# Kernel tuning notes

Hardware: AMD Instinct MI355X
Metric: run time of the kernel (lower is better)

Reference implementation:

```python
import jax, jax.numpy as jnp
import numpy as np

N_NODES = 100000


def gcn_layer(x, row, col, W, b, n):
    # x: [N, Fin] -> h: [N, Fout]
    h = x @ W + b
    deg = jax.ops.segment_sum(jnp.ones_like(row, dtype=h.dtype), row, num_segments=n)
    dis = deg ** -0.5  # deg >= 1 thanks to self loops
    norm = dis[row] * dis[col]          # [E]
    msg = norm[:, None] * h[row]        # gather + scale
    return jax.ops.segment_sum(msg, col, num_segments=n)  # scatter-add to targets


def setup_inputs() -> dict:
    key = jax.random.key(0)
    k1, k2, k3, k4, k5, k6 = jax.random.split(key, 6)
    x = jax.random.normal(k1, (N_NODES, 512), dtype=jnp.float32)
    edge_index = jax.random.randint(k2, (2, 3200000), 0, N_NODES, dtype=jnp.int32)
    W1 = jax.random.normal(k3, (512, 16), dtype=jnp.float32) * 0.05
    b1 = jax.random.normal(k4, (16,), dtype=jnp.float32) * 0.05
    W2 = jax.random.normal(k5, (16, 40), dtype=jnp.float32) * 0.05
    b2 = jax.random.normal(k6, (40,), dtype=jnp.float32) * 0.05
    return {"x": x, "edge_index": edge_index, "W1": W1, "b1": b1, "W2": W2, "b2": b2}


def reference(x, edge_index, W1, b1, W2, b2):
    n = x.shape[0]
    # add_self_loops
    loops = jnp.arange(n, dtype=edge_index.dtype)
    row = jnp.concatenate([edge_index[0], loops])
    col = jnp.concatenate([edge_index[1], loops])
    h = gcn_layer(x, row, col, W1, b1, n)
    h = jax.nn.relu(h)
    # F.dropout with training=False (eval) is identity
    h = gcn_layer(h, row, col, W2, b2, n)
    return jax.nn.log_softmax(h, axis=1)
```

## Files before the change

### kernel.cpp

```cpp
#include <hip/hip_runtime.h>
#include <math.h>

#define N_NODES 100000
#define N_EDGES 3200000
#define F_IN    512
#define F1      16
#define F2      40

#define N_BUCKETS 6250
#define CAP       768

#define BR 256
#define KK 32
#define XPITCH 36

__global__ __launch_bounds__(256, 4) void mm1_kernel(
        const float* __restrict__ x, const float* __restrict__ W1,
        const float* __restrict__ b1, const float* __restrict__ dis,
        float* __restrict__ h1t) {
    __shared__ float xs[BR * XPITCH];
    __shared__ float ws[KK * F1];
    int t = threadIdx.x;
    int rbase = blockIdx.x * BR;
    int jq = t & 3;
    int rg = t >> 2;
    float acc[4][4];
#pragma unroll
    for (int i = 0; i < 4; ++i)
#pragma unroll
        for (int j = 0; j < 4; ++j) acc[i][j] = 0.0f;

    for (int ch = 0; ch < F_IN / KK; ++ch) {
        int c0 = ch * KK;
#pragma unroll
        for (int i = 0; i < 8; ++i) {
            int p  = t + i * 256;
            int tr = p >> 3;
            int f4 = p & 7;
            float4 v = make_float4(0.0f, 0.0f, 0.0f, 0.0f);
            int grow = rbase + tr;
            if (grow < N_NODES)
                v = *(const float4*)(x + (size_t)grow * F_IN + c0 + f4 * 4);
            *(float4*)&xs[tr * XPITCH + f4 * 4] = v;
        }
        if (t < 128) {
            int kk = t >> 2, f4 = t & 3;
            *(float4*)&ws[kk * F1 + f4 * 4] =
                *(const float4*)(W1 + (size_t)(c0 + kk) * F1 + f4 * 4);
        }
        __syncthreads();
#pragma unroll
        for (int k4 = 0; k4 < KK / 4; ++k4) {
            float xa[4][4], wa[4][4];
#pragma unroll
            for (int i = 0; i < 4; ++i)
                *(float4*)&xa[i][0] =
                    *(const float4*)&xs[(rg * 4 + i) * XPITCH + k4 * 4];
#pragma unroll
            for (int m = 0; m < 4; ++m)
                *(float4*)&wa[m][0] =
                    *(const float4*)&ws[(k4 * 4 + m) * F1 + jq * 4];
#pragma unroll
            for (int i = 0; i < 4; ++i)
#pragma unroll
                for (int m = 0; m < 4; ++m)
#pragma unroll
                    for (int j = 0; j < 4; ++j)
                        acc[i][j] = fmaf(xa[i][m], wa[m][j], acc[i][j]);
        }
        __syncthreads();
    }

    float4 bv = *(const float4*)(b1 + jq * 4);
#pragma unroll
    for (int i = 0; i < 4; ++i) {
        int grow = rbase + rg * 4 + i;
        if (grow < N_NODES) {
            float d = dis[grow];
            float4 o;
            o.x = d * (acc[i][0] + bv.x);
            o.y = d * (acc[i][1] + bv.y);
            o.z = d * (acc[i][2] + bv.z);
            o.w = d * (acc[i][3] + bv.w);
            *(float4*)(h1t + (size_t)grow * F1 + jq * 4) = o;
        }
    }
}

__global__ void init_kernel(int* __restrict__ bcur_c, int* __restrict__ bcur_r) {
    int i = blockIdx.x * blockDim.x + threadIdx.x;
    if (i < N_BUCKETS) { bcur_c[i] = 0; bcur_r[i] = 0; }
}

__global__ void bin_kernel(const int* __restrict__ row, const int* __restrict__ col,
                           int* __restrict__ bcur_c, int* __restrict__ bcur_r,
                           int* __restrict__ staging_c, unsigned char* __restrict__ staging_r) {
    int e = blockIdx.x * blockDim.x + threadIdx.x;
    if (e >= N_EDGES) return;
    int r = row[e];
    int c = col[e];
    int bc = c >> 4;
    int pc = atomicAdd(&bcur_c[bc], 1);
    if (pc < CAP) staging_c[bc * CAP + pc] = r | ((c & 15) << 27);
    int br = r >> 4;
    int pr = atomicAdd(&bcur_r[br], 1);
    if (pr < CAP) staging_r[br * CAP + pr] = (unsigned char)(r & 15);
}

__global__ void deg_kernel(const unsigned char* __restrict__ staging_r,
                           const int* __restrict__ bcur_r, float* __restrict__ dis) {
    __shared__ int cnt16[16];
    int b = blockIdx.x, t = threadIdx.x;
    if (t < 16) cnt16[t] = 0;
    __syncthreads();
    int size = min(bcur_r[b], CAP);
    const unsigned char* sb = staging_r + (size_t)b * CAP;
    for (int k = t; k < size; k += 256)
        atomicAdd(&cnt16[sb[k]], 1);
    __syncthreads();
    if (t < 16) dis[b * 16 + t] = rsqrtf((float)(cnt16[t] + 1));
}

__global__ void scanb_kernel(const int* __restrict__ bcur_c, int* __restrict__ bucket_start) {
    __shared__ int lds[256];
    int t = threadIdx.x;
    int base = t * 25;
    int s = 0;
    for (int i = 0; i < 25; ++i) {
        int idx = base + i;
        if (idx < N_BUCKETS) s += min(bcur_c[idx], CAP);
    }
    lds[t] = s;
    __syncthreads();
    for (int off = 1; off < 256; off <<= 1) {
        int v = (t >= off) ? lds[t - off] : 0;
        __syncthreads();
        lds[t] += v;
        __syncthreads();
    }
    int run = lds[t] - s;
    for (int i = 0; i < 25; ++i) {
        int idx = base + i;
        if (idx < N_BUCKETS) {
            bucket_start[idx] = run;
            run += min(bcur_c[idx], CAP);
        }
    }
}

__global__ void csr_kernel(const int* __restrict__ staging_c, const int* __restrict__ bcur_c,
                           const int* __restrict__ bucket_start,
                           int* __restrict__ start, int* __restrict__ cnt,
                           int* __restrict__ rows_sorted) {
    __shared__ int cnt16[16], off16[16], cur16[16];
    int b = blockIdx.x, t = threadIdx.x;
    if (t < 16) cnt16[t] = 0;
    __syncthreads();
    int size = min(bcur_c[b], CAP);
    const int* sb = staging_c + (size_t)b * CAP;
    for (int k = t; k < size; k += 256)
        atomicAdd(&cnt16[(sb[k] >> 27) & 15], 1);
    __syncthreads();
    if (t == 0) {
        int s = 0;
#pragma unroll
        for (int i = 0; i < 16; ++i) { off16[i] = s; s += cnt16[i]; }
    }
    __syncthreads();
    int base = bucket_start[b];
    if (t < 16) {
        start[b * 16 + t] = base + off16[t];
        cnt[b * 16 + t]   = cnt16[t];
        cur16[t] = 0;
    }
    __syncthreads();
    for (int k = t; k < size; k += 256) {
        int entry = sb[k];
        int c4 = (entry >> 27) & 15;
        int pos = atomicAdd(&cur16[c4], 1);
        rows_sorted[base + off16[c4] + pos] = entry & 0x07FFFFFF;
    }
}

__global__ void agg1_kernel(const int* __restrict__ rows_sorted,
                            const int* __restrict__ start, const int* __restrict__ cnt,
                            const float* __restrict__ dis, const float* __restrict__ h1t,
                            float* __restrict__ g, float* __restrict__ s_out) {
    int idx = blockIdx.x * blockDim.x + threadIdx.x;
    if (idx >= N_NODES * 4) return;
    int c = idx >> 2;
    int q = idx & 3;
    float dc = dis[c];
    const float4* h4 = (const float4*)h1t;
    float4 acc = h4[(size_t)c * 4 + q];
    float ss = dc;
    int k0 = start[c];
    int k1 = k0 + cnt[c];
    for (int k = k0; k < k1; ++k) {
        int r = rows_sorted[k];
        float4 v = h4[(size_t)r * 4 + q];
        acc.x += v.x; acc.y += v.y; acc.z += v.z; acc.w += v.w;
        if (q == 0) ss += dis[r];
    }
    acc.x = dc * fmaxf(acc.x * dc, 0.0f);
    acc.y = dc * fmaxf(acc.y * dc, 0.0f);
    acc.z = dc * fmaxf(acc.z * dc, 0.0f);
    acc.w = dc * fmaxf(acc.w * dc, 0.0f);
    ((float4*)g)[(size_t)c * 4 + q] = acc;
    if (q == 0) s_out[c] = dc * ss;
}

__global__ void agg2_kernel(const int* __restrict__ rows_sorted,
                            const int* __restrict__ start, const int* __restrict__ cnt,
                            const float* __restrict__ dis, const float* __restrict__ g,
                            float* __restrict__ t) {
    int idx = blockIdx.x * blockDim.x + threadIdx.x;
    if (idx >= N_NODES * 4) return;
    int c = idx >> 2;
    int q = idx & 3;
    float dc = dis[c];
    const float4* h4 = (const float4*)g;
    float4 acc = h4[(size_t)c * 4 + q];
    int k0 = start[c];
    int k1 = k0 + cnt[c];
    for (int k = k0; k < k1; ++k) {
        int r = rows_sorted[k];
        float4 v = h4[(size_t)r * 4 + q];
        acc.x += v.x; acc.y += v.y; acc.z += v.z; acc.w += v.w;
    }
    acc.x *= dc; acc.y *= dc; acc.z *= dc; acc.w *= dc;
    ((float4*)t)[(size_t)c * 4 + q] = acc;
}

__global__ void mm2lsm_kernel(const float* __restrict__ t, const float* __restrict__ s,
                              const float* __restrict__ W2, const float* __restrict__ b2,
                              float* __restrict__ out) {
    __shared__ float w2s[F1 * F2];
    __shared__ float b2s[F2];
    __shared__ float ts[4 * F1];
    int tid = threadIdx.x;
    for (int i = tid; i < F1 * F2; i += 256) w2s[i] = W2[i];
    if (tid < F2) b2s[tid] = b2[tid];
    int nodeBase = blockIdx.x * 4;
    if (tid < 4 * F1) ts[tid] = t[(size_t)nodeBase * F1 + tid];
    __syncthreads();
    int w    = tid >> 6;
    int lane = tid & 63;
    int c = nodeBase + w;
    float sc = s[c];
    float v = -INFINITY;
    if (lane < F2) {
        float acc = sc * b2s[lane];
#pragma unroll
        for (int k = 0; k < F1; ++k)
            acc = fmaf(ts[w * F1 + k], w2s[k * F2 + lane], acc);
        v = acc;
    }
    float m = v;
#pragma unroll
    for (int off = 32; off; off >>= 1)
        m = fmaxf(m, __shfl_xor(m, off, 64));
    float ex = (lane < F2) ? expf(v - m) : 0.0f;
    float ssum = ex;
#pragma unroll
    for (int off = 32; off; off >>= 1)
        ssum += __shfl_xor(ssum, off, 64);
    if (lane < F2) out[(size_t)c * F2 + lane] = v - m - logf(ssum);
}

extern "C" void kernel_launch(void* const* d_in, const int* in_sizes, int n_in,
                              void* d_out, int out_size, void* d_ws, size_t ws_size,
                              hipStream_t stream) {
    const float* x   = (const float*)d_in[0];
    const int*   ei  = (const int*)d_in[1];
    const float* W1  = (const float*)d_in[2];
    const float* b1  = (const float*)d_in[3];
    const float* W2  = (const float*)d_in[4];
    const float* b2  = (const float*)d_in[5];
    float* out = (float*)d_out;

    const int* row = ei;
    const int* col = ei + N_EDGES;

    const size_t P = 102400;
    float* fws = (float*)d_ws;
    float* dis = fws;
    float* s   = dis + P;
    int* start = (int*)(s + P);
    int* cnt   = start + P;
    int* bucket_start = cnt + P;
    int* bcur_c       = bucket_start + 8192;
    int* bcur_r       = bcur_c + 8192;
    int* rows_sorted  = bcur_r + 8192;
    int* staging_c    = rows_sorted + N_EDGES;
    float* h1t = (float*)staging_c;
    float* t   = (float*)staging_c + 16 * P;
    unsigned char* staging_r = (unsigned char*)(staging_c + (size_t)N_BUCKETS * CAP);
    float* g = (float*)staging_r;

    const int B = 256;
    const int gridE = (N_EDGES + B - 1) / B;

    init_kernel<<<(N_BUCKETS + B - 1) / B, B, 0, stream>>>(bcur_c, bcur_r);
    bin_kernel<<<gridE, B, 0, stream>>>(row, col, bcur_c, bcur_r, staging_c, staging_r);
    deg_kernel<<<N_BUCKETS, B, 0, stream>>>(staging_r, bcur_r, dis);
    scanb_kernel<<<1, 256, 0, stream>>>(bcur_c, bucket_start);
    csr_kernel<<<N_BUCKETS, B, 0, stream>>>(staging_c, bcur_c, bucket_start,
                                            start, cnt, rows_sorted);

    mm1_kernel<<<(N_NODES + BR - 1) / BR, B, 0, stream>>>(x, W1, b1, dis, h1t);
    agg1_kernel<<<(N_NODES * 4 + B - 1) / B, B, 0, stream>>>(
        rows_sorted, start, cnt, dis, h1t, g, s);

    agg2_kernel<<<(N_NODES * 4 + B - 1) / B, B, 0, stream>>>(
        rows_sorted, start, cnt, dis, g, t);

    mm2lsm_kernel<<<N_NODES / 4, B, 0, stream>>>(t, s, W2, b2, out);
}
```

Before: 880.0 us.

## Partition edge binning into sub-buckets and count degrees with direct atomics

Edge binning by target-node bucket now spreads its atomic cursors over 8 partitions per bucket, chosen by block index, with an overflow area, so fewer threads contend on the same counter. Degree counting drops the separate row-bucket staging pass and its kernel and uses one atomicAdd per edge on a per-node array plus a small rsqrt kernel. The scan and CSR build walk the partitioned layout. Capacities are fixed per partition (120) and for overflow (32), so heavily skewed inputs could drop edges.

After: 877.0 us. About the same (-0.3%).

```diff
diff --git a/kernel.cpp b/kernel.cpp
--- a/kernel.cpp
+++ b/kernel.cpp
@@ -8,7 +8,9 @@
 #define F2      40
 
 #define N_BUCKETS 6250
-#define CAP       768
+#define NPART     8
+#define CAPP      120
+#define OCAP      32
 
 #define BR 256
 #define KK 32
@@ -87,48 +89,55 @@
     }
 }
 
-__global__ void init_kernel(int* __restrict__ bcur_c, int* __restrict__ bcur_r) {
+__global__ void init_kernel(int* __restrict__ deg, int* __restrict__ bcur,
+                            int* __restrict__ ocur) {
     int i = blockIdx.x * blockDim.x + threadIdx.x;
-    if (i < N_BUCKETS) { bcur_c[i] = 0; bcur_r[i] = 0; }
+    if (i < N_NODES) deg[i] = 0;
+    if (i < N_BUCKETS * NPART) bcur[i] = 0;
+    if (i < N_BUCKETS) ocur[i] = 0;
 }
 
 __global__ void bin_kernel(const int* __restrict__ row, const int* __restrict__ col,
-                           int* __restrict__ bcur_c, int* __restrict__ bcur_r,
-                           int* __restrict__ staging_c, unsigned char* __restrict__ staging_r) {
+                           int* __restrict__ deg,
+                           int* __restrict__ bcur, int* __restrict__ ocur,
+                           int* __restrict__ staging, int* __restrict__ staging_o) {
     int e = blockIdx.x * blockDim.x + threadIdx.x;
     if (e >= N_EDGES) return;
+    int part = blockIdx.x & (NPART - 1);
     int r = row[e];
     int c = col[e];
+    atomicAdd(&deg[r], 1);
     int bc = c >> 4;
-    int pc = atomicAdd(&bcur_c[bc], 1);
-    if (pc < CAP) staging_c[bc * CAP + pc] = r | ((c & 15) << 27);
-    int br = r >> 4;
-    int pr = atomicAdd(&bcur_r[br], 1);
-    if (pr < CAP) staging_r[br * CAP + pr] = (unsigned char)(r & 15);
-}
-
-__global__ void deg_kernel(const unsigned char* __restrict__ staging_r,
-                           const int* __restrict__ bcur_r, float* __restrict__ dis) {
-    __shared__ int cnt16[16];
-    int b = blockIdx.x, t = threadIdx.x;
-    if (t < 16) cnt16[t] = 0;
-    __syncthreads();
-    int size = min(bcur_r[b], CAP);
-    const unsigned char* sb = staging_r + (size_t)b * CAP;
-    for (int k = t; k < size; k += 256)
-        atomicAdd(&cnt16[sb[k]], 1);
-    __syncthreads();
-    if (t < 16) dis[b * 16 + t] = rsqrtf((float)(cnt16[t] + 1));
-}
-
-__global__ void scanb_kernel(const int* __restrict__ bcur_c, int* __restrict__ bucket_start) {
+    int payload = r | ((c & 15) << 27);
+    int cell = bc * NPART + part;
+    int pc = atomicAdd(&bcur[cell], 1);
+    if (pc < CAPP) {
+        staging[(size_t)cell * CAPP + pc] = payload;
+    } else {
+        int po = atomicAdd(&ocur[bc], 1);
+        if (po < OCAP) staging_o[(size_t)bc * OCAP + po] = payload;
+    }
+}
+
+__global__ void dis_kernel(const int* __restrict__ deg, float* __restrict__ dis) {
+    int i = blockIdx.x * blockDim.x + threadIdx.x;
+    if (i < N_NODES) dis[i] = rsqrtf((float)(deg[i] + 1));
+}
+
+__global__ void scanb_kernel(const int* __restrict__ bcur, const int* __restrict__ ocur,
+                             int* __restrict__ bucket_start) {
     __shared__ int lds[256];
     int t = threadIdx.x;
     int base = t * 25;
     int s = 0;
     for (int i = 0; i < 25; ++i) {
         int idx = base + i;
-        if (idx < N_BUCKETS) s += min(bcur_c[idx], CAP);
+        if (idx < N_BUCKETS) {
+            int tot = min(ocur[idx], OCAP);
+#pragma unroll
+            for (int p = 0; p < NPART; ++p) tot += min(bcur[idx * NPART + p], CAPP);
+            s += tot;
+        }
     }
     lds[t] = s;
     __syncthreads();
@@ -143,12 +152,16 @@
         int idx = base + i;
         if (idx < N_BUCKETS) {
             bucket_start[idx] = run;
-            run += min(bcur_c[idx], CAP);
-        }
-    }
-}
-
-__global__ void csr_kernel(const int* __restrict__ staging_c, const int* __restrict__ bcur_c,
+            int tot = min(ocur[idx], OCAP);
+#pragma unroll
+            for (int p = 0; p < NPART; ++p) tot += min(bcur[idx * NPART + p], CAPP);
+            run += tot;
+        }
+    }
+}
+
+__global__ void csr_kernel(const int* __restrict__ staging, const int* __restrict__ staging_o,
+                           const int* __restrict__ bcur, const int* __restrict__ ocur,
                            const int* __restrict__ bucket_start,
                            int* __restrict__ start, int* __restrict__ cnt,
                            int* __restrict__ rows_sorted) {
@@ -156,10 +169,18 @@
     int b = blockIdx.x, t = threadIdx.x;
     if (t < 16) cnt16[t] = 0;
     __syncthreads();
-    int size = min(bcur_c[b], CAP);
-    const int* sb = staging_c + (size_t)b * CAP;
-    for (int k = t; k < size; k += 256)
-        atomicAdd(&cnt16[(sb[k] >> 27) & 15], 1);
+    const int* sb = staging + (size_t)b * NPART * CAPP;
+    int szs[NPART];
+#pragma unroll
+    for (int p = 0; p < NPART; ++p) szs[p] = min(bcur[b * NPART + p], CAPP);
+    int szo = min(ocur[b], OCAP);
+    const int* so = staging_o + (size_t)b * OCAP;
+#pragma unroll
+    for (int p = 0; p < NPART; ++p)
+        for (int k = t; k < szs[p]; k += 256)
+            atomicAdd(&cnt16[(sb[p * CAPP + k] >> 27) & 15], 1);
+    for (int k = t; k < szo; k += 256)
+        atomicAdd(&cnt16[(so[k] >> 27) & 15], 1);
     __syncthreads();
     if (t == 0) {
         int s = 0;
@@ -174,8 +195,16 @@
         cur16[t] = 0;
     }
     __syncthreads();
-    for (int k = t; k < size; k += 256) {
-        int entry = sb[k];
+#pragma unroll
+    for (int p = 0; p < NPART; ++p)
+        for (int k = t; k < szs[p]; k += 256) {
+            int entry = sb[p * CAPP + k];
+            int c4 = (entry >> 27) & 15;
+            int pos = atomicAdd(&cur16[c4], 1);
+            rows_sorted[base + off16[c4] + pos] = entry & 0x07FFFFFF;
+        }
+    for (int k = t; k < szo; k += 256) {
+        int entry = so[k];
         int c4 = (entry >> 27) & 15;
         int pos = atomicAdd(&cur16[c4], 1);
         rows_sorted[base + off16[c4] + pos] = entry & 0x07FFFFFF;
@@ -288,25 +317,26 @@
     float* s   = dis + P;
     int* start = (int*)(s + P);
     int* cnt   = start + P;
-    int* bucket_start = cnt + P;
-    int* bcur_c       = bucket_start + 8192;
-    int* bcur_r       = bcur_c + 8192;
-    int* rows_sorted  = bcur_r + 8192;
-    int* staging_c    = rows_sorted + N_EDGES;
-    float* h1t = (float*)staging_c;
-    float* t   = (float*)staging_c + 16 * P;
-    unsigned char* staging_r = (unsigned char*)(staging_c + (size_t)N_BUCKETS * CAP);
-    float* g = (float*)staging_r;
+    int* deg   = cnt + P;
+    int* bucket_start = deg + P;
+    int* bcur  = bucket_start + 8192;
+    int* ocur  = bcur + 51200;
+    int* rows_sorted = ocur + 8192;
+    int* staging_o   = rows_sorted + N_EDGES;
+    int* staging     = staging_o + (size_t)N_BUCKETS * OCAP;
+    float* h1t = (float*)staging;
+    float* t   = (float*)staging + 16 * P;
+    float* g   = (float*)staging + 32 * P;
 
     const int B = 256;
     const int gridE = (N_EDGES + B - 1) / B;
 
-    init_kernel<<<(N_BUCKETS + B - 1) / B, B, 0, stream>>>(bcur_c, bcur_r);
-    bin_kernel<<<gridE, B, 0, stream>>>(row, col, bcur_c, bcur_r, staging_c, staging_r);
-    deg_kernel<<<N_BUCKETS, B, 0, stream>>>(staging_r, bcur_r, dis);
-    scanb_kernel<<<1, 256, 0, stream>>>(bcur_c, bucket_start);
-    csr_kernel<<<N_BUCKETS, B, 0, stream>>>(staging_c, bcur_c, bucket_start,
-                                            start, cnt, rows_sorted);
+    init_kernel<<<(int)((P + B - 1) / B), B, 0, stream>>>(deg, bcur, ocur);
+    bin_kernel<<<gridE, B, 0, stream>>>(row, col, deg, bcur, ocur, staging, staging_o);
+    dis_kernel<<<(N_NODES + B - 1) / B, B, 0, stream>>>(deg, dis);
+    scanb_kernel<<<1, 256, 0, stream>>>(bcur, ocur, bucket_start);
+    csr_kernel<<<N_BUCKETS, B, 0, stream>>>(staging, staging_o, bcur, ocur,
+                                            bucket_start, start, cnt, rows_sorted);
 
     mm1_kernel<<<(N_NODES + BR - 1) / BR, B, 0, stream>>>(x, W1, b1, dis, h1t);
     agg1_kernel<<<(N_NODES * 4 + B - 1) / B, B, 0, stream>>>(
```

## Replace fine-grained atomic binning with LDS-buffered coarse buckets and XCC-partitioned degrees

Applied to the files above, without the earlier changes.

Edge binning now groups destinations into 196 coarse buckets of 512 nodes. Each workgroup buffers entries in LDS and flushes them to global staging as full 64-byte lines, with overflow going to a small stash. Degrees are counted with per-XCC partitioned global atomics and summed in a separate kernel. The per-bucket CSR build now runs as one large-LDS workgroup per coarse bucket, which removes the separate scan kernel and the byte-staging degree pass. In exchange, the CSR stage has low parallelism (196 blocks) and every block scans the whole stash. Buckets that overflow their capacity could silently drop edges.

New measurement: 889.6 us. About the same (+1.1%).

```diff
diff --git a/kernel.cpp b/kernel.cpp
--- a/kernel.cpp
+++ b/kernel.cpp
@@ -7,12 +7,22 @@
 #define F1      16
 #define F2      40
 
-#define N_BUCKETS 6250
-#define CAP       768
+#define NB1    196
+#define BDEPTH 32
+#define CAP1   21536
+#define CAPR   17664
+#define NWG1   512
+#define STASH  4096
 
 #define BR 256
 #define KK 32
 #define XPITCH 36
+
+__device__ __forceinline__ int xcc_id() {
+    unsigned x;
+    asm volatile("s_getreg_b32 %0, hwreg(HW_REG_XCC_ID)" : "=s"(x));
+    return (int)(x & 7);
+}
 
 __global__ __launch_bounds__(256, 4) void mm1_kernel(
         const float* __restrict__ x, const float* __restrict__ W1,
@@ -87,99 +97,170 @@
     }
 }
 
-__global__ void init_kernel(int* __restrict__ bcur_c, int* __restrict__ bcur_r) {
+__global__ void init_kernel(int* __restrict__ deg8, int* __restrict__ gcur1,
+                            int* __restrict__ oscur) {
     int i = blockIdx.x * blockDim.x + threadIdx.x;
-    if (i < N_BUCKETS) { bcur_c[i] = 0; bcur_r[i] = 0; }
-}
-
-__global__ void bin_kernel(const int* __restrict__ row, const int* __restrict__ col,
-                           int* __restrict__ bcur_c, int* __restrict__ bcur_r,
-                           int* __restrict__ staging_c, unsigned char* __restrict__ staging_r) {
-    int e = blockIdx.x * blockDim.x + threadIdx.x;
-    if (e >= N_EDGES) return;
-    int r = row[e];
-    int c = col[e];
-    int bc = c >> 4;
-    int pc = atomicAdd(&bcur_c[bc], 1);
-    if (pc < CAP) staging_c[bc * CAP + pc] = r | ((c & 15) << 27);
-    int br = r >> 4;
-    int pr = atomicAdd(&bcur_r[br], 1);
-    if (pr < CAP) staging_r[br * CAP + pr] = (unsigned char)(r & 15);
-}
-
-__global__ void deg_kernel(const unsigned char* __restrict__ staging_r,
-                           const int* __restrict__ bcur_r, float* __restrict__ dis) {
-    __shared__ int cnt16[16];
+    if (i < 8 * 102400) deg8[i] = 0;
+    if (i < NB1) gcur1[i] = 0;
+    if (i == 0) *oscur = 0;
+}
+
+__global__ __launch_bounds__(256) void bin_kernel(
+        const int* __restrict__ row, const int* __restrict__ col,
+        int* __restrict__ deg8, int* __restrict__ gcur1, int* __restrict__ oscur,
+        int2* __restrict__ stash, int* __restrict__ staging1) {
+    __shared__ int buf1[NB1][BDEPTH];
+    __shared__ int cur1[NB1];
+    __shared__ int myBase[NB1];
+    __shared__ short flushList[2 * NB1];
+    __shared__ int flushCnt;
+    int t = threadIdx.x;
+    int part = xcc_id();
+    for (int i = t; i < NB1; i += 256) cur1[i] = 0;
+    if (t == 0) flushCnt = 0;
+    __syncthreads();
+    const int chunk = N_EDGES / NWG1;
+    int e0 = blockIdx.x * chunk;
+    const int nbatch = (chunk + 255) / 256;
+    for (int batch = 0; batch <= nbatch; ++batch) {
+        if (batch < nbatch) {
+            int e = e0 + batch * 256 + t;
+            if (e < e0 + chunk) {
+                int r = row[e];
+                int c = col[e];
+                atomicAdd(&deg8[part * 102400 + r], 1);
+                int p1 = r | ((c & 511) << 17);
+                int bb = c >> 9;
+                int pos = atomicAdd(&cur1[bb], 1);
+                if (pos < BDEPTH) buf1[bb][pos] = p1;
+                else { int sp = atomicAdd(oscur, 1);
+                       if (sp < STASH) stash[sp] = make_int2(bb, p1); }
+            }
+        } else {
+            if (t < NB1) {
+                int rem = min(cur1[t], BDEPTH);
+                if (rem & 15) {
+                    int up = (rem + 15) & ~15;
+                    for (int i = rem; i < up; ++i) buf1[t][i] = -1;
+                    cur1[t] = up;
+                }
+            }
+        }
+        __syncthreads();
+        if (t < NB1) {
+            int n = min(cur1[t], BDEPTH);
+            int lines = n >> 4;
+            if (lines) {
+                int base = atomicAdd(&gcur1[t], lines * 16);
+                if (base + lines * 16 <= CAP1) {
+                    myBase[t] = base;
+                    int li = atomicAdd(&flushCnt, lines);
+                    for (int L = 0; L < lines; ++L)
+                        flushList[li + L] = (short)((t << 2) | L);
+                } else {
+                    for (int i = 0; i < lines * 16; ++i) {
+                        int sp = atomicAdd(oscur, 1);
+                        if (sp < STASH) stash[sp] = make_int2(t, buf1[t][i]);
+                    }
+                }
+            }
+        }
+        __syncthreads();
+        int fc = flushCnt;
+        for (int j = t; j < fc * 4; j += 256) {
+            int g = flushList[j >> 2];
+            int lane4 = j & 3;
+            int bb = g >> 2, L = g & 3;
+            int4 v = *(int4*)&buf1[bb][L * 16 + lane4 * 4];
+            *(int4*)&staging1[(size_t)bb * CAP1 + myBase[bb] + L * 16 + lane4 * 4] = v;
+        }
+        __syncthreads();
+        if (t < NB1) {
+            int n = min(cur1[t], BDEPTH);
+            int lines = n >> 4, rem = n & 15;
+            if (lines) for (int i = 0; i < rem; ++i) buf1[t][i] = buf1[t][lines * 16 + i];
+            cur1[t] = rem;
+        }
+        if (t == 0) flushCnt = 0;
+        __syncthreads();
+    }
+}
+
+__global__ void dis_kernel(const int* __restrict__ deg8, float* __restrict__ dis) {
+    int i = blockIdx.x * blockDim.x + threadIdx.x;
+    if (i < N_NODES) {
+        int d = 1;
+#pragma unroll
+        for (int p = 0; p < 8; ++p) d += deg8[p * 102400 + i];
+        dis[i] = rsqrtf((float)d);
+    }
+}
+
+__global__ __launch_bounds__(256) void csr2_kernel(
+        const int* __restrict__ staging1, const int* __restrict__ gcur1,
+        const int* __restrict__ oscur, const int2* __restrict__ stash,
+        int* __restrict__ start, int* __restrict__ cnt,
+        int* __restrict__ rows_sorted) {
+    __shared__ int ebuf[CAPR];
+    __shared__ int cnt512[512], off512[512], cur512[512];
+    __shared__ int psum[256];
     int b = blockIdx.x, t = threadIdx.x;
-    if (t < 16) cnt16[t] = 0;
-    __syncthreads();
-    int size = min(bcur_r[b], CAP);
-    const unsigned char* sb = staging_r + (size_t)b * CAP;
-    for (int k = t; k < size; k += 256)
-        atomicAdd(&cnt16[sb[k]], 1);
-    __syncthreads();
-    if (t < 16) dis[b * 16 + t] = rsqrtf((float)(cnt16[t] + 1));
-}
-
-__global__ void scanb_kernel(const int* __restrict__ bcur_c, int* __restrict__ bucket_start) {
-    __shared__ int lds[256];
-    int t = threadIdx.x;
-    int base = t * 25;
-    int s = 0;
-    for (int i = 0; i < 25; ++i) {
-        int idx = base + i;
-        if (idx < N_BUCKETS) s += min(bcur_c[idx], CAP);
-    }
-    lds[t] = s;
+    for (int i = t; i < 512; i += 256) { cnt512[i] = 0; cur512[i] = 0; }
+    __syncthreads();
+    const int* sb = staging1 + (size_t)b * CAP1;
+    int n1 = min(gcur1[b], CAP1);
+    for (int k = t; k < n1; k += 256) {
+        int e = sb[k];
+        if (e != -1) atomicAdd(&cnt512[(e >> 17) & 511], 1);
+    }
+    int ns = min(*oscur, STASH);
+    for (int k = t; k < ns; k += 256) {
+        int2 se = stash[k];
+        if (se.x == b && se.y != -1) atomicAdd(&cnt512[(se.y >> 17) & 511], 1);
+    }
+    __syncthreads();
+    int a0 = cnt512[2 * t], a1 = cnt512[2 * t + 1];
+    int ps = a0 + a1;
+    psum[t] = ps;
     __syncthreads();
     for (int off = 1; off < 256; off <<= 1) {
-        int v = (t >= off) ? lds[t - off] : 0;
-        __syncthreads();
-        lds[t] += v;
-        __syncthreads();
-    }
-    int run = lds[t] - s;
-    for (int i = 0; i < 25; ++i) {
-        int idx = base + i;
-        if (idx < N_BUCKETS) {
-            bucket_start[idx] = run;
-            run += min(bcur_c[idx], CAP);
-        }
-    }
-}
-
-__global__ void csr_kernel(const int* __restrict__ staging_c, const int* __restrict__ bcur_c,
-                           const int* __restrict__ bucket_start,
-                           int* __restrict__ start, int* __restrict__ cnt,
-                           int* __restrict__ rows_sorted) {
-    __shared__ int cnt16[16], off16[16], cur16[16];
-    int b = blockIdx.x, t = threadIdx.x;
-    if (t < 16) cnt16[t] = 0;
-    __syncthreads();
-    int size = min(bcur_c[b], CAP);
-    const int* sb = staging_c + (size_t)b * CAP;
-    for (int k = t; k < size; k += 256)
-        atomicAdd(&cnt16[(sb[k] >> 27) & 15], 1);
-    __syncthreads();
-    if (t == 0) {
-        int s = 0;
-#pragma unroll
-        for (int i = 0; i < 16; ++i) { off16[i] = s; s += cnt16[i]; }
-    }
-    __syncthreads();
-    int base = bucket_start[b];
-    if (t < 16) {
-        start[b * 16 + t] = base + off16[t];
-        cnt[b * 16 + t]   = cnt16[t];
-        cur16[t] = 0;
-    }
-    __syncthreads();
-    for (int k = t; k < size; k += 256) {
-        int entry = sb[k];
-        int c4 = (entry >> 27) & 15;
-        int pos = atomicAdd(&cur16[c4], 1);
-        rows_sorted[base + off16[c4] + pos] = entry & 0x07FFFFFF;
-    }
+        int v = (t >= off) ? psum[t - off] : 0;
+        __syncthreads();
+        psum[t] += v;
+        __syncthreads();
+    }
+    int excl = psum[t] - ps;
+    off512[2 * t] = excl;
+    off512[2 * t + 1] = excl + a0;
+    __syncthreads();
+    for (int i = t; i < 512; i += 256) {
+        int node = b * 512 + i;
+        start[node] = b * CAPR + off512[i];
+        cnt[node]   = cnt512[i];
+    }
+    for (int k = t; k < n1; k += 256) {
+        int e = sb[k];
+        if (e != -1) {
+            int i = (e >> 17) & 511;
+            int pos = atomicAdd(&cur512[i], 1);
+            int dst = off512[i] + pos;
+            if (dst < CAPR) ebuf[dst] = e & 0x1FFFF;
+        }
+    }
+    for (int k = t; k < ns; k += 256) {
+        int2 se = stash[k];
+        if (se.x == b && se.y != -1) {
+            int i = (se.y >> 17) & 511;
+            int pos = atomicAdd(&cur512[i], 1);
+            int dst = off512[i] + pos;
+            if (dst < CAPR) ebuf[dst] = se.y & 0x1FFFF;
+        }
+    }
+    __syncthreads();
+    int total = off512[511] + cnt512[511];
+    if (total > CAPR) total = CAPR;
+    int* out = rows_sorted + (size_t)b * CAPR;
+    for (int k = t; k < total; k += 256) out[k] = ebuf[k];
 }
 
 __global__ void agg1_kernel(const int* __restrict__ rows_sorted,
@@ -288,25 +369,23 @@
     float* s   = dis + P;
     int* start = (int*)(s + P);
     int* cnt   = start + P;
-    int* bucket_start = cnt + P;
-    int* bcur_c       = bucket_start + 8192;
-    int* bcur_r       = bcur_c + 8192;
-    int* rows_sorted  = bcur_r + 8192;
-    int* staging_c    = rows_sorted + N_EDGES;
-    float* h1t = (float*)staging_c;
-    float* t   = (float*)staging_c + 16 * P;
-    unsigned char* staging_r = (unsigned char*)(staging_c + (size_t)N_BUCKETS * CAP);
-    float* g = (float*)staging_r;
+    int* gcur1 = cnt + P;
+    int* oscur = gcur1 + 256;
+    int2* stash = (int2*)(oscur + 8);
+    int* rows_sorted = (int*)(oscur + 8) + 2 * STASH;
+    int* deg8 = rows_sorted;
+    int* staging1 = rows_sorted + (size_t)NB1 * CAPR;
+    float* h1t = (float*)staging1;
+    float* t   = (float*)staging1 + 16 * P;
+    float* g   = (float*)(staging1 + (size_t)NB1 * CAP1);
 
     const int B = 256;
-    const int gridE = (N_EDGES + B - 1) / B;
-
-    init_kernel<<<(N_BUCKETS + B - 1) / B, B, 0, stream>>>(bcur_c, bcur_r);
-    bin_kernel<<<gridE, B, 0, stream>>>(row, col, bcur_c, bcur_r, staging_c, staging_r);
-    deg_kernel<<<N_BUCKETS, B, 0, stream>>>(staging_r, bcur_r, dis);
-    scanb_kernel<<<1, 256, 0, stream>>>(bcur_c, bucket_start);
-    csr_kernel<<<N_BUCKETS, B, 0, stream>>>(staging_c, bcur_c, bucket_start,
-                                            start, cnt, rows_sorted);
+
+    init_kernel<<<(8 * (int)P + B - 1) / B, B, 0, stream>>>(deg8, gcur1, oscur);
+    bin_kernel<<<NWG1, B, 0, stream>>>(row, col, deg8, gcur1, oscur, stash, staging1);
+    dis_kernel<<<(N_NODES + B - 1) / B, B, 0, stream>>>(deg8, dis);
+    csr2_kernel<<<NB1, B, 0, stream>>>(staging1, gcur1, oscur, stash,
+                                       start, cnt, rows_sorted);
 
     mm1_kernel<<<(N_NODES + BR - 1) / BR, B, 0, stream>>>(x, W1, b1, dis, h1t);
     agg1_kernel<<<(N_NODES * 4 + B - 1) / B, B, 0, stream>>>(
```
